# Optimization experiments

Measured on AMD Instinct MI355X. Metric: run time of the kernel, lower is better.

## Reference

```python
import jax, jax.numpy as jnp
import numpy as np

H = 128
EPS = 1e-5

def _lstm_layer(x, Wih, Whh, bih, bhh):
    # x: [B,T,D] -> h_seq: [B,T,H]. PyTorch gate order: i,f,g,o.
    xw = jnp.einsum('btd,gd->btg', x, Wih) + bih + bhh  # [B,T,4H]
    B = x.shape[0]
    h0 = jnp.zeros((B, H), x.dtype)
    c0 = jnp.zeros((B, H), x.dtype)
    def step(carry, xt):
        h, c = carry
        gates = xt + h @ Whh.T  # [B,4H]
        i, f, g, o = jnp.split(gates, 4, axis=-1)
        i = jax.nn.sigmoid(i); f = jax.nn.sigmoid(f)
        g = jnp.tanh(g); o = jax.nn.sigmoid(o)
        c = f * c + i * g
        h = o * jnp.tanh(c)
        return (h, c), h
    _, hs = jax.lax.scan(step, (h0, c0), jnp.swapaxes(xw, 0, 1))  # [T,B,H]
    return jnp.swapaxes(hs, 0, 1)

def setup_inputs() -> dict:
    key = jax.random.key(0)
    ks = jax.random.split(key, 16)
    B, T, D = 1024, 512, 14
    s = 1.0 / np.sqrt(H)
    u = lambda k, shp: jax.random.uniform(k, shp, jnp.float32, -s, s)
    return {
        'x': jax.random.normal(ks[0], (B, T, D), jnp.float32),
        'Wih0': u(ks[1], (4 * H, D)), 'Whh0': u(ks[2], (4 * H, H)),
        'bih0': u(ks[3], (4 * H,)), 'bhh0': u(ks[4], (4 * H,)),
        'Wih1': u(ks[5], (4 * H, H)), 'Whh1': u(ks[6], (4 * H, H)),
        'bih1': u(ks[7], (4 * H,)), 'bhh1': u(ks[8], (4 * H,)),
        'gamma': jnp.ones((H,), jnp.float32), 'beta': jnp.zeros((H,), jnp.float32),
        'W1': u(ks[9], (32, H)), 'b1': u(ks[10], (32,)),
        'W2': u(ks[11], (1, 32)), 'b2': u(ks[12], (1,)),
    }

def reference(x, Wih0, Whh0, bih0, bhh0, Wih1, Whh1, bih1, bhh1,
              gamma, beta, W1, b1, W2, b2):
    h1 = _lstm_layer(x, Wih0, Whh0, bih0, bhh0)   # [B,T,H] (inter-layer dropout off: eval)
    h2 = _lstm_layer(h1, Wih1, Whh1, bih1, bhh1)  # [B,T,H]
    last = h2[:, -1, :]                            # [B,H]
    mu = jnp.mean(last, axis=0)
    var = jnp.mean((last - mu) ** 2, axis=0)       # biased, matching torch BN
    normalized = (last - mu) / jnp.sqrt(var + EPS) * gamma + beta
    z = jax.nn.relu(normalized @ W1.T + b1)        # dropout identity in eval
    out = z @ W2.T + b2                            # [B,1]
    return out.squeeze(-1)
```

## Files before the change

kernel.cpp:

```cpp
#include <hip/hip_runtime.h>


#define B_ 1024
#define T_ 512
#define D_ 14
#define H_ 128
#define NB 4
#define NT 512

#define L2E 1.44269504088896f
#define L2E2 2.88539008177793f

typedef _Float16 f16;
typedef _Float16 half4 __attribute__((ext_vector_type(4)));
typedef _Float16 half8 __attribute__((ext_vector_type(8)));
typedef _Float16 f16x2 __attribute__((ext_vector_type(2)));
typedef float floatx4 __attribute__((ext_vector_type(4)));

__device__ __forceinline__ half8 ldfrag_s(const float* __restrict__ p, float s) {
    half8 r;
#pragma unroll
    for (int j = 0; j < 8; ++j) r[j] = (f16)(p[j] * s);
    return r;
}

#define MFMA(a, b, c) __builtin_amdgcn_mfma_f32_16x16x32_f16((a), (b), (c), 0, 0, 0)

__device__ __forceinline__ float cellP(float pi, float pf, float pg, float po, float& cs)
{
    float a = __builtin_amdgcn_exp2f(-pi);
    float u = __builtin_amdgcn_exp2f(-pf);
    float b = __builtin_amdgcn_exp2f(pg);
    float d = __builtin_amdgcn_exp2f(-po);
    float t1 = 1.0f + a;
    float t3 = 1.0f + u;
    float t2 = __builtin_fmaf(t1, b, t1);
    float bm = b - 1.0f;
    float num = __builtin_fmaf(L2E2 * bm, t3, cs * t2);
    cs = num * __builtin_amdgcn_rcpf(t2 * t3);
    float e = __builtin_amdgcn_exp2f(cs);
    float t4 = 1.0f + d;
    float t5 = __builtin_fmaf(t4, e, t4);
    return (e - 1.0f) * __builtin_amdgcn_rcpf(t5);
}

__global__ __launch_bounds__(NT, 1) void lstm_fused(
    const float* __restrict__ x,
    const float* __restrict__ Wih0, const float* __restrict__ Whh0,
    const float* __restrict__ bih0, const float* __restrict__ bhh0,
    const float* __restrict__ Wih1, const float* __restrict__ Whh1,
    const float* __restrict__ bih1, const float* __restrict__ bhh1,
    float* __restrict__ h2last)
{
    __shared__ __align__(16) f16 whh1lds[8][4][2][64][8];
    __shared__ __align__(16) f16 h1f[2][4][64][8];
    __shared__ __align__(16) f16 h2f[2][4][64][8];
    __shared__ __align__(16) f16 xf[2][64][8];

    const int tid = threadIdx.x;
    const int lane = tid & 63;
    const int wv = tid >> 6;
    const int n = lane & 15;
    const int q = lane >> 4;
    const int b0 = blockIdx.x * NB;

    {
        unsigned int* z1 = (unsigned int*)h1f;
        unsigned int* z2 = (unsigned int*)h2f;
#pragma unroll
        for (int i = 0; i < 4; ++i) {
            z1[tid + i * 512] = 0u;
            z2[tid + i * 512] = 0u;
        }
        ((unsigned int*)xf)[tid] = 0u;
    }
    __syncthreads();

    if (tid < NB) {
        xf[0][tid + 16][7] = (f16)1.0f;
        xf[1][tid + 16][7] = (f16)1.0f;
    }
    if (tid < 64) {
        int nn = tid & 15, kq = tid >> 4;
        if (nn < NB && kq < 2) {
            half8 v;
#pragma unroll
            for (int e = 0; e < 8; ++e) {
                int k = kq * 8 + e;
                v[e] = (k < D_) ? (f16)x[(size_t)(b0 + nn) * T_ * D_ + k]
                                : (k == 15 ? (f16)1.0f : (f16)0.0f);
            }
            *(half8*)&xf[0][tid][0] = v;
        }
    }

    const float* xpp = x + (size_t)(b0 + (tid & 3)) * T_ * D_ + D_ + (tid >> 2);

    const int wg = wv;
    half8 aWhh0[4][4], aWih0[4];
    half8 aWih1[4][4], aWhh1r[4][2];
    f16x2 b1p[4][2];
#pragma unroll
    for (int g = 0; g < 4; ++g) {
        const float gs = (g == 2) ? L2E2 : L2E;
        const int gr = g * 128 + wg * 16 + n;
#pragma unroll
        for (int kt = 0; kt < 4; ++kt)
            aWhh0[g][kt] = ldfrag_s(Whh0 + (size_t)gr * H_ + kt * 32 + q * 8, gs);
        half8 w0;
#pragma unroll
        for (int e = 0; e < 8; ++e) {
            int k = q * 8 + e;
            if (k < D_)       w0[e] = (f16)(Wih0[(size_t)gr * D_ + k] * gs);
            else if (k == 15) w0[e] = (f16)((bih0[gr] + bhh0[gr]) * gs);
            else              w0[e] = (f16)0.0f;
        }
        aWih0[g] = w0;
#pragma unroll
        for (int kt = 0; kt < 4; ++kt) {
            aWih1[g][kt] = ldfrag_s(Wih1 + (size_t)gr * H_ + kt * 32 + q * 8, gs);
            half8 wf = ldfrag_s(Whh1 + (size_t)gr * H_ + kt * 32 + q * 8, gs);
            if (kt < 2) aWhh1r[g][kt] = wf;
            else        *(half8*)&whh1lds[wg][g][kt - 2][lane][0] = wf;
        }
        const int gb = g * 128 + wg * 16 + q * 4;
        f16x2 p0, p1;
        p0[0] = (f16)((bih1[gb]     + bhh1[gb])     * gs);
        p0[1] = (f16)((bih1[gb + 1] + bhh1[gb + 1]) * gs);
        p1[0] = (f16)((bih1[gb + 2] + bhh1[gb + 2]) * gs);
        p1[1] = (f16)((bih1[gb + 3] + bhh1[gb + 3]) * gs);
        b1p[g][0] = p0;
        b1p[g][1] = p1;
    }

    floatx4 cs1 = {0.f, 0.f, 0.f, 0.f};
    floatx4 cs2 = {0.f, 0.f, 0.f, 0.f};
    __syncthreads();

    for (int p = 0; p <= T_; ++p) {
        const int cur = p & 1, nxt = cur ^ 1;
        const bool doA = (p < T_);
        const bool doB = (p >= 1);

        float xp = 0.0f;
        if (tid < NB * D_ && (p + 1) < T_) xp = *xpp;

        floatx4 C0[4], C1[4];
#pragma unroll
        for (int g = 0; g < 4; ++g) {
            C0[g] = floatx4{0.f, 0.f, 0.f, 0.f};
            C1[g] = floatx4{0.f, 0.f, 0.f, 0.f};
        }

        if (doA) {
            half8 bx = *(const half8*)&xf[cur][lane][0];
#pragma unroll
            for (int g = 0; g < 4; ++g) C0[g] = MFMA(aWih0[g], bx, C0[g]);
        }
#pragma unroll
        for (int kt = 0; kt < 4; ++kt) {
            half8 bh = *(const half8*)&h1f[cur][kt][lane][0];
            if (doA) {
#pragma unroll
                for (int g = 0; g < 4; ++g) C0[g] = MFMA(aWhh0[g][kt], bh, C0[g]);
            }
            if (doB) {
#pragma unroll
                for (int g = 0; g < 4; ++g) C1[g] = MFMA(aWih1[g][kt], bh, C1[g]);
            }
        }
        if (doB) {
#pragma unroll
            for (int kt = 0; kt < 2; ++kt) {
                half8 bh = *(const half8*)&h2f[cur][kt][lane][0];
#pragma unroll
                for (int g = 0; g < 4; ++g) C1[g] = MFMA(aWhh1r[g][kt], bh, C1[g]);
            }
#pragma unroll
            for (int kt = 2; kt < 4; ++kt) {
                half8 bh = *(const half8*)&h2f[cur][kt][lane][0];
#pragma unroll
                for (int g = 0; g < 4; ++g) {
                    half8 aw = *(const half8*)&whh1lds[wg][g][kt - 2][lane][0];
                    C1[g] = MFMA(aw, bh, C1[g]);
                }
            }
        }

        const int ktw = wg >> 1;
        const int qw = (wg & 1) * 2 + (q >> 1);
        const int eb = (q & 1) * 4;
        if (doA) {
            half4 hp;
#pragma unroll
            for (int r = 0; r < 4; ++r) {
                float c = cs1[r];
                hp[r] = (f16)cellP(C0[0][r], C0[1][r], C0[2][r], C0[3][r], c);
                cs1[r] = c;
            }
            if (n < NB) *(half4*)&h1f[nxt][ktw][n + 16 * qw][eb] = hp;
        }
        if (doB) {
            half4 hp;
            floatx4 hv;
#pragma unroll
            for (int r = 0; r < 4; ++r) {
                float pi = C1[0][r] + (float)b1p[0][r >> 1][r & 1];
                float pf = C1[1][r] + (float)b1p[1][r >> 1][r & 1];
                float pg = C1[2][r] + (float)b1p[2][r >> 1][r & 1];
                float po = C1[3][r] + (float)b1p[3][r >> 1][r & 1];
                float c = cs2[r];
                hv[r] = cellP(pi, pf, pg, po, c);
                cs2[r] = c;
                hp[r] = (f16)hv[r];
            }
            if (n < NB) {
                *(half4*)&h2f[nxt][ktw][n + 16 * qw][eb] = hp;
                if (p == T_) {
#pragma unroll
                    for (int r = 0; r < 4; ++r)
                        h2last[(size_t)(b0 + n) * H_ + wg * 16 + q * 4 + r] = hv[r];
                }
            }
        }
        if (tid < NB * D_ && (p + 1) < T_) {
            int k = tid >> 2;
            xf[nxt][(tid & 3) + 16 * (k >> 3)][k & 7] = (f16)xp;
            xpp += D_;
        }
        __syncthreads();
    }
}

__global__ void bn_stats(const float* __restrict__ h2last, float* __restrict__ stats)
{
    __shared__ float red[2][8][128];
    const int tid = threadIdx.x;
    const int j = tid & 127, bs = tid >> 7;
    float s = 0.0f, ss = 0.0f;
    for (int bb = 0; bb < 128; ++bb) {
        float v = h2last[(size_t)(bb * 8 + bs) * H_ + j];
        s += v;
        ss += v * v;
    }
    red[0][bs][j] = s;
    red[1][bs][j] = ss;
    __syncthreads();
    if (tid < 128) {
        float S = 0.0f, SS = 0.0f;
#pragma unroll
        for (int k = 0; k < 8; ++k) { S += red[0][k][tid]; SS += red[1][k][tid]; }
        float mu = S * (1.0f / 1024.0f);
        float var = SS * (1.0f / 1024.0f) - mu * mu;
        stats[tid] = mu;
        stats[128 + tid] = __builtin_amdgcn_rsqf(var + 1e-5f);
    }
}

__global__ void bn_mlp(const float* __restrict__ h2last, const float* __restrict__ stats,
                       const float* __restrict__ gamma, const float* __restrict__ beta,
                       const float* __restrict__ W1, const float* __restrict__ b1,
                       const float* __restrict__ W2, const float* __restrict__ b2,
                       float* __restrict__ out)
{
    __shared__ float W1T[128][33];
    __shared__ float mus[128], isds[128], gs[128], bts[128], w2s[32];
    const int tid = threadIdx.x;
    const int b = blockIdx.x * 128 + tid;

    for (int i = tid; i < 4096; i += 128) {
        int k = i >> 7, j = i & 127;
        W1T[j][k] = W1[i];
    }
    mus[tid] = stats[tid];
    isds[tid] = stats[128 + tid];
    gs[tid] = gamma[tid];
    bts[tid] = beta[tid];
    if (tid < 32) w2s[tid] = W2[tid];
    __syncthreads();

    float z[32];
#pragma unroll
    for (int k = 0; k < 32; ++k) z[k] = b1[k];

    for (int j = 0; j < 128; ++j) {
        float nv = (h2last[(size_t)b * H_ + j] - mus[j]) * isds[j] * gs[j] + bts[j];
#pragma unroll
        for (int k = 0; k < 32; ++k) z[k] += W1T[j][k] * nv;
    }
    float o = b2[0];
#pragma unroll
    for (int k = 0; k < 32; ++k) o += w2s[k] * fmaxf(z[k], 0.0f);
    out[b] = o;
}

extern "C" void kernel_launch(void* const* d_in, const int* in_sizes, int n_in,
                              void* d_out, int out_size, void* d_ws, size_t ws_size,
                              hipStream_t stream)
{
    const float* x    = (const float*)d_in[0];
    const float* Wih0 = (const float*)d_in[1];
    const float* Whh0 = (const float*)d_in[2];
    const float* bih0 = (const float*)d_in[3];
    const float* bhh0 = (const float*)d_in[4];
    const float* Wih1 = (const float*)d_in[5];
    const float* Whh1 = (const float*)d_in[6];
    const float* bih1 = (const float*)d_in[7];
    const float* bhh1 = (const float*)d_in[8];
    const float* gamma = (const float*)d_in[9];
    const float* beta  = (const float*)d_in[10];
    const float* W1 = (const float*)d_in[11];
    const float* b1 = (const float*)d_in[12];
    const float* W2 = (const float*)d_in[13];
    const float* b2 = (const float*)d_in[14];

    float* h2last = (float*)d_ws;
    float* stats  = h2last + (size_t)B_ * H_;
    float* out = (float*)d_out;

    hipLaunchKernelGGL(lstm_fused, dim3(B_ / NB), dim3(NT), 0, stream,
                       x, Wih0, Whh0, bih0, bhh0, Wih1, Whh1, bih1, bhh1, h2last);
    hipLaunchKernelGGL(bn_stats, dim3(1), dim3(1024), 0, stream, h2last, stats);
    hipLaunchKernelGGL(bn_mlp, dim3(8), dim3(128), 0, stream,
                       h2last, stats, gamma, beta, W1, b1, W2, b2, out);
}
```

Measured before the change: 1.073 ms.

## Redistribute LSTM cell updates across all lanes via LDS transpose

```diff
diff --git a/kernel.cpp b/kernel.cpp
--- a/kernel.cpp
+++ b/kernel.cpp
@@ -56,6 +56,8 @@
     __shared__ __align__(16) f16 h1f[2][4][64][8];
     __shared__ __align__(16) f16 h2f[2][4][64][8];
     __shared__ __align__(16) f16 xf[2][64][8];
+    __shared__ __align__(16) float credA[8][4][4][16];
+    __shared__ __align__(16) float credB[8][4][4][16];
 
     const int tid = threadIdx.x;
     const int lane = tid & 63;
@@ -81,13 +83,13 @@
         xf[1][tid + 16][7] = (f16)1.0f;
     }
     if (tid < 64) {
-        int nn = tid & 15, kq = tid >> 4;
-        if (nn < NB && kq < 2) {
+        int nn_ = tid & 15, kq = tid >> 4;
+        if (nn_ < NB && kq < 2) {
             half8 v;
 #pragma unroll
             for (int e = 0; e < 8; ++e) {
                 int k = kq * 8 + e;
-                v[e] = (k < D_) ? (f16)x[(size_t)(b0 + nn) * T_ * D_ + k]
+                v[e] = (k < D_) ? (f16)x[(size_t)(b0 + nn_) * T_ * D_ + k]
                                 : (k == 15 ? (f16)1.0f : (f16)0.0f);
             }
             *(half8*)&xf[0][tid][0] = v;
@@ -99,7 +101,6 @@
     const int wg = wv;
     half8 aWhh0[4][4], aWih0[4];
     half8 aWih1[4][4], aWhh1r[4][2];
-    f16x2 b1p[4][2];
 #pragma unroll
     for (int g = 0; g < 4; ++g) {
         const float gs = (g == 2) ? L2E2 : L2E;
@@ -123,18 +124,24 @@
             if (kt < 2) aWhh1r[g][kt] = wf;
             else        *(half8*)&whh1lds[wg][g][kt - 2][lane][0] = wf;
         }
-        const int gb = g * 128 + wg * 16 + q * 4;
-        f16x2 p0, p1;
-        p0[0] = (f16)((bih1[gb]     + bhh1[gb])     * gs);
-        p0[1] = (f16)((bih1[gb + 1] + bhh1[gb + 1]) * gs);
-        p1[0] = (f16)((bih1[gb + 2] + bhh1[gb + 2]) * gs);
-        p1[1] = (f16)((bih1[gb + 3] + bhh1[gb + 3]) * gs);
-        b1p[g][0] = p0;
-        b1p[g][1] = p1;
-    }
-
-    floatx4 cs1 = {0.f, 0.f, 0.f, 0.f};
-    floatx4 cs2 = {0.f, 0.f, 0.f, 0.f};
+    }
+
+    const int jj = lane & 15;
+    const int nn = lane >> 4;
+    const int qD = jj >> 2, rD = jj & 3;
+    const int ktD = wg >> 1;
+    const int rowD = nn + 16 * ((wg & 1) * 2 + (qD >> 1));
+    const int eD = (qD & 1) * 4 + rD;
+    float bias1v[4];
+#pragma unroll
+    for (int g = 0; g < 4; ++g) {
+        const float gs = (g == 2) ? L2E2 : L2E;
+        const int gb = g * 128 + wg * 16 + jj;
+        bias1v[g] = (bih1[gb] + bhh1[gb]) * gs;
+    }
+
+    float cs1 = 0.0f;
+    float cs2 = 0.0f;
     __syncthreads();
 
     for (int p = 0; p <= T_; ++p) {
@@ -152,6 +159,7 @@
             C1[g] = floatx4{0.f, 0.f, 0.f, 0.f};
         }
 
+        __builtin_amdgcn_s_setprio(1);
         if (doA) {
             half8 bx = *(const half8*)&xf[cur][lane][0];
 #pragma unroll
@@ -186,43 +194,42 @@
                 }
             }
         }
-
-        const int ktw = wg >> 1;
-        const int qw = (wg & 1) * 2 + (q >> 1);
-        const int eb = (q & 1) * 4;
+        __builtin_amdgcn_s_setprio(0);
+
         if (doA) {
-            half4 hp;
-#pragma unroll
-            for (int r = 0; r < 4; ++r) {
-                float c = cs1[r];
-                hp[r] = (f16)cellP(C0[0][r], C0[1][r], C0[2][r], C0[3][r], c);
-                cs1[r] = c;
-            }
-            if (n < NB) *(half4*)&h1f[nxt][ktw][n + 16 * qw][eb] = hp;
-        }
+            if (n < NB) {
+#pragma unroll
+                for (int g = 0; g < 4; ++g)
+                    *(floatx4*)&credA[wv][g][n][q * 4] = C0[g];
+            }
+            asm volatile("s_waitcnt lgkmcnt(0)" ::: "memory");
+            __builtin_amdgcn_sched_barrier(0);
+            float g0 = credA[wv][0][nn][jj];
+            float g1 = credA[wv][1][nn][jj];
+            float g2 = credA[wv][2][nn][jj];
+            float g3 = credA[wv][3][nn][jj];
+            float h0 = cellP(g0, g1, g2, g3, cs1);
+            h1f[nxt][ktD][rowD][eD] = (f16)h0;
+        }
+
         if (doB) {
-            half4 hp;
-            floatx4 hv;
-#pragma unroll
-            for (int r = 0; r < 4; ++r) {
-                float pi = C1[0][r] + (float)b1p[0][r >> 1][r & 1];
-                float pf = C1[1][r] + (float)b1p[1][r >> 1][r & 1];
-                float pg = C1[2][r] + (float)b1p[2][r >> 1][r & 1];
-                float po = C1[3][r] + (float)b1p[3][r >> 1][r & 1];
-                float c = cs2[r];
-                hv[r] = cellP(pi, pf, pg, po, c);
-                cs2[r] = c;
-                hp[r] = (f16)hv[r];
-            }
             if (n < NB) {
-                *(half4*)&h2f[nxt][ktw][n + 16 * qw][eb] = hp;
-                if (p == T_) {
-#pragma unroll
-                    for (int r = 0; r < 4; ++r)
-                        h2last[(size_t)(b0 + n) * H_ + wg * 16 + q * 4 + r] = hv[r];
-                }
-            }
-        }
+#pragma unroll
+                for (int g = 0; g < 4; ++g)
+                    *(floatx4*)&credB[wv][g][n][q * 4] = C1[g];
+            }
+            asm volatile("s_waitcnt lgkmcnt(0)" ::: "memory");
+            __builtin_amdgcn_sched_barrier(0);
+            float g0 = credB[wv][0][nn][jj] + bias1v[0];
+            float g1 = credB[wv][1][nn][jj] + bias1v[1];
+            float g2 = credB[wv][2][nn][jj] + bias1v[2];
+            float g3 = credB[wv][3][nn][jj] + bias1v[3];
+            float hv = cellP(g0, g1, g2, g3, cs2);
+            h2f[nxt][ktD][rowD][eD] = (f16)hv;
+            if (p == T_)
+                h2last[(size_t)(b0 + nn) * H_ + wg * 16 + jj] = hv;
+        }
+
         if (tid < NB * D_ && (p + 1) < T_) {
             int k = tid >> 2;
             xf[nxt][(tid & 3) + 16 * (k >> 3)][k & 7] = (f16)xp;
```

New measurement: 968.9 us. 1.11x faster.
